# Kernel optimization log

Measured on AMD Instinct MI355X. Metric: run time of the kernel, lower is better.

## Reference

```python
import jax, jax.numpy as jnp
import numpy as np

N, E, ND, ED, H, L = 50000, 800000, 64, 32, 128, 4
MIN = 2 * H + H + 1  # message MLP input dim = 385
EPS = 1e-5


def _layernorm(x, w, b):
    mu = x.mean(-1, keepdims=True)
    var = ((x - mu) ** 2).mean(-1, keepdims=True)
    return (x - mu) / jnp.sqrt(var + EPS) * w + b


def setup_inputs() -> dict:
    key = jax.random.key(0)
    ks = jax.random.split(key, 40)

    def w(k, shape):
        return jax.random.normal(k, shape, jnp.float32) / np.sqrt(shape[-2]).astype(np.float32)

    inp = {
        "node_features": jax.random.normal(ks[0], (N, ND), jnp.float32),
        "edge_features": jax.random.normal(ks[1], (E, ED), jnp.float32),
        "congestion": jax.random.uniform(ks[2], (N,), jnp.float32),
        "edge_index": jax.random.randint(ks[3], (2, E), 0, N),
        "unrouted_mask": jax.random.randint(ks[4], (N,), 0, 2).astype(jnp.bool_),
        "enc_node_w": w(ks[5], (ND, H)), "enc_node_b": jnp.zeros(H),
        "enc_edge_w": w(ks[6], (ED, H)), "enc_edge_b": jnp.zeros(H),
        "msg_w1": w(ks[7], (L, MIN, H)), "msg_b1": jnp.zeros((L, H)),
        "msg_w2": w(ks[8], (L, H, H)), "msg_b2": jnp.zeros((L, H)),
        "upd_w1": w(ks[9], (L, 2 * H, H)), "upd_b1": jnp.zeros((L, H)),
        "upd_w2": w(ks[10], (L, H, H)), "upd_b2": jnp.zeros((L, H)),
        "ln_w": jnp.ones((L, H)), "ln_b": jnp.zeros((L, H)),
        "unr_w1": w(ks[11], (1, H)), "unr_b1": jnp.zeros(H),
        "unr_w2": w(ks[12], (H, H)), "unr_b2": jnp.zeros(H),
        "ro_w1": w(ks[13], (2 * H, H)), "ro_b1": jnp.zeros(H),
        "ro_w2": w(ks[14], (H, H // 2)), "ro_b2": jnp.zeros(H // 2),
        "ro_w3": w(ks[15], (H // 2, 1)), "ro_b3": jnp.zeros(1),
    }
    return inp


def reference(node_features, edge_features, congestion, edge_index, unrouted_mask,
              enc_node_w, enc_node_b, enc_edge_w, enc_edge_b,
              msg_w1, msg_b1, msg_w2, msg_b2,
              upd_w1, upd_b1, upd_w2, upd_b2,
              ln_w, ln_b,
              unr_w1, unr_b1, unr_w2, unr_b2,
              ro_w1, ro_b1, ro_w2, ro_b2, ro_w3, ro_b3):
    n = node_features.shape[0]
    src, dst = edge_index[0], edge_index[1]

    x = node_features @ enc_node_w + enc_node_b            # [N, H]
    ea = edge_features @ enc_edge_w + enc_edge_b           # [E, H]
    cong_src = congestion[src][:, None]                    # [E, 1]

    for l in range(msg_w1.shape[0]):
        # message: gather src/dst features, concat with edge attr + congestion
        m_in = jnp.concatenate([x[src], x[dst], ea, cong_src], axis=-1)  # [E, 385]
        m = jax.nn.relu(m_in @ msg_w1[l] + msg_b1[l]) @ msg_w2[l] + msg_b2[l]  # [E, H]
        agg = jax.ops.segment_sum(m, dst, num_segments=n)  # scatter_add over dst
        u_in = jnp.concatenate([x, agg], axis=-1)          # [N, 2H]
        x_new = jax.nn.relu(u_in @ upd_w1[l] + upd_b1[l]) @ upd_w2[l] + upd_b2[l]
        x = _layernorm(x + x_new, ln_w[l], ln_b[l])        # dropout = identity (eval)

    graph_embed = x.mean(axis=0, keepdims=True)            # [1, H] (batch=None branch)
    unrouted_frac = unrouted_mask.astype(jnp.float32).mean()[None, None]  # [1, 1]
    unr = jax.nn.relu(unrouted_frac @ unr_w1 + unr_b1) @ unr_w2 + unr_b2  # [1, H]
    combined = jnp.concatenate([graph_embed, unr], axis=-1)  # [1, 2H]
    h = jax.nn.relu(combined @ ro_w1 + ro_b1)
    h = jax.nn.relu(h @ ro_w2 + ro_b2)
    out = jax.nn.sigmoid(h @ ro_w3 + ro_b3)                # [1, 1]
    return out.squeeze(-1)                                 # [1]
```

## Files before the change

### kernel.cpp

```cpp
#include <hip/hip_runtime.h>
#include <hip/hip_fp16.h>
#include <math.h>

#define NN 50000
#define EE 800000

typedef _Float16 half8 __attribute__((ext_vector_type(8)));
typedef __fp16 fp16x2 __attribute__((ext_vector_type(2)));
typedef float floatx4 __attribute__((ext_vector_type(4)));

__global__ void fold_kernel(const float* __restrict__ ew, const float* __restrict__ eb,
                            const float* __restrict__ w1, const float* __restrict__ b1,
                            float* __restrict__ Wc, float* __restrict__ b1f) {
  int l = blockIdx.y, c = blockIdx.x, j = threadIdx.x;
  __shared__ float row[128];
  const float* w1l = w1 + (size_t)l * 385 * 128;
  if (c < 32) {
    row[j] = ew[c * 128 + j];
    __syncthreads();
    float acc = 0.f;
    for (int k = 0; k < 128; k++) acc += row[k] * w1l[(256 + k) * 128 + j];
    Wc[((size_t)l * 32 + c) * 128 + j] = acc;
  } else {
    row[j] = eb[j];
    __syncthreads();
    float acc = b1[l * 128 + j];
    for (int k = 0; k < 128; k++) acc += row[k] * w1l[(256 + k) * 128 + j];
    b1f[l * 128 + j] = acc;
  }
}

__global__ void prep_w(const float* __restrict__ src, _Float16* __restrict__ dst,
                       int K, int perm) {
  int l = blockIdx.y;
  int lane = threadIdx.x;
  int kc = blockIdx.x >> 3, nt = blockIdx.x & 7;
  int n = nt * 16 + (lane & 15);
  int k0 = kc * 32 + (lane >> 4) * 8;
  const float* s = src + (size_t)l * K * 128;
  _Float16 out[8];
  for (int j = 0; j < 8; j++) {
    int k = k0 + j;
    int ks = perm ? ((k & 7) * 16 + (k >> 3)) : k;
    out[j] = (_Float16)s[(size_t)ks * 128 + n];
  }
  _Float16* d = dst + (((size_t)l * gridDim.x + blockIdx.x) * 64 + lane) * 8;
  *(half8*)d = *(half8*)out;
}

__global__ void prep_cong(const float* __restrict__ mw1, _Float16* __restrict__ w1cp) {
  int l = blockIdx.x, p = threadIdx.x;
  int col = (p & 7) * 16 + (p >> 3);
  w1cp[l * 128 + p] = (_Float16)mw1[((size_t)l * 385 + 384) * 128 + col];
}

__global__ void hist_kernel(const int* __restrict__ dstv, int* __restrict__ counts,
                            int* __restrict__ rank) {
  int e = blockIdx.x * 256 + threadIdx.x;
  if (e < EE) rank[e] = atomicAdd(&counts[dstv[e]], 1);
}

__global__ void scan1_kernel(const int* __restrict__ counts, int* __restrict__ offs,
                             int* __restrict__ bsum) {
  __shared__ int ws[16];
  int t = threadIdx.x, lane = t & 63, w = t >> 6;
  int i = blockIdx.x * 1024 + t;
  int v = (i < NN) ? counts[i] : 0;
  int s = v;
  for (int off = 1; off < 64; off <<= 1) {
    int u = __shfl_up(s, off);
    if (lane >= off) s += u;
  }
  if (lane == 63) ws[w] = s;
  __syncthreads();
  if (w == 0) {
    int u = (lane < 16) ? ws[lane] : 0;
    for (int off = 1; off < 16; off <<= 1) {
      int x = __shfl_up(u, off);
      if (lane >= off && lane < 16) u += x;
    }
    if (lane < 16) ws[lane] = u;
  }
  __syncthreads();
  int wbase = (w > 0) ? ws[w - 1] : 0;
  if (i < NN) offs[i] = wbase + s - v;
  if (t == 0) bsum[blockIdx.x] = ws[15];
}

__global__ void scan2_kernel(int* __restrict__ bsum) {
  int t = threadIdx.x;
  int v = (t < 49) ? bsum[t] : 0;
  int s = v;
  for (int off = 1; off < 64; off <<= 1) {
    int u = __shfl_up(s, off);
    if (t >= off) s += u;
  }
  if (t < 49) bsum[t] = s - v;
}

__global__ void slot1_kernel(const int* __restrict__ dstv, const int* __restrict__ offs,
                             const int* __restrict__ bsum, const int* __restrict__ rank,
                             int* __restrict__ einv) {
  int e = blockIdx.x * 256 + threadIdx.x;
  if (e >= EE) return;
  int d = dstv[e];
  int p = offs[d] + bsum[d >> 10] + rank[e];
  einv[p] = e;
}

__global__ void slot2_kernel(const int* __restrict__ einv, const int* __restrict__ srcv,
                             const int* __restrict__ dstv, const float* __restrict__ ef,
                             int2* __restrict__ meta, _Float16* __restrict__ efh) {
  int p = blockIdx.x * 256 + threadIdx.x;
  if (p >= EE) return;
  int e = einv[p];
  int2 m;
  m.x = srcv[e];
  m.y = dstv[e];
  meta[p] = m;
  const float* sp = ef + (size_t)e * 32;
  _Float16* dp = efh + (size_t)p * 32;
  for (int i = 0; i < 4; i++) {
    float4 f = *(const float4*)(sp + i * 8);
    float4 g = *(const float4*)(sp + i * 8 + 4);
    half8 v;
    v[0] = (_Float16)f.x; v[1] = (_Float16)f.y; v[2] = (_Float16)f.z; v[3] = (_Float16)f.w;
    v[4] = (_Float16)g.x; v[5] = (_Float16)g.y; v[6] = (_Float16)g.z; v[7] = (_Float16)g.w;
    *(half8*)(dp + i * 8) = v;
  }
}

__global__ void enc_mfma(const float* __restrict__ nf, const _Float16* __restrict__ Wenc,
                         const float* __restrict__ bn, _Float16* __restrict__ xh,
                         const _Float16* __restrict__ WSa, const _Float16* __restrict__ WSb,
                         const float* __restrict__ b1f,
                         _Float16* __restrict__ Sh, _Float16* __restrict__ Dh,
                         _Float16* __restrict__ aggz,
                         const int* __restrict__ um, float* __restrict__ red) {
  __shared__ __align__(16) _Float16 hs[4][16][136];
  int t = threadIdx.x, wave = t >> 6, lane = t & 63;
  int quad = lane >> 4, l15 = lane & 15;
  long nb0 = (long)blockIdx.x * 64 + wave * 16;
  long rn = nb0 + l15;
  if (rn >= NN) rn = NN - 1;

  {
    long zn = (long)blockIdx.x * 64 + (t >> 2);
    if (zn < NN) {
      float4* p = (float4*)(aggz + (long)blockIdx.x * 64 * 128 + t * 32);
      float4 z = {};
      p[0] = z; p[1] = z; p[2] = z; p[3] = z;
    }
  }

  if (t < 64) {
    long n = (long)blockIdx.x * 64 + t;
    float mv = (n < NN) ? (float)um[n] : 0.f;
    for (int off = 32; off; off >>= 1) mv += __shfl_xor(mv, off);
    if (t == 0) atomicAdd(&red[128], mv);
  }

  floatx4 acc[8] = {};
  for (int kc = 0; kc < 2; kc++) {
    const float* p = nf + rn * 64 + kc * 32 + quad * 8;
    float4 f0 = *(const float4*)p;
    float4 f1 = *(const float4*)(p + 4);
    half8 a;
    a[0] = (_Float16)f0.x; a[1] = (_Float16)f0.y;
    a[2] = (_Float16)f0.z; a[3] = (_Float16)f0.w;
    a[4] = (_Float16)f1.x; a[5] = (_Float16)f1.y;
    a[6] = (_Float16)f1.z; a[7] = (_Float16)f1.w;
    const _Float16* bp = Wenc + (size_t)(kc * 8) * 512 + lane * 8;
    for (int nt = 0; nt < 8; nt++) {
      half8 b = *(const half8*)(bp + nt * 512);
      acc[nt] = __builtin_amdgcn_mfma_f32_16x16x32_f16(a, b, acc[nt], 0, 0, 0);
    }
  }
  float bv[8];
  for (int nt = 0; nt < 8; nt++) bv[nt] = bn[nt * 16 + l15];
  for (int reg = 0; reg < 4; reg++) {
    long n = nb0 + quad * 4 + reg;
    bool ok = n < NN;
    for (int nt = 0; nt < 8; nt++) {
      _Float16 v = (_Float16)(acc[nt][reg] + bv[nt]);
      if (ok) xh[n * 128 + nt * 16 + l15] = v;
      hs[wave][quad * 4 + reg][nt * 16 + l15] = v;
    }
  }

  {
    floatx4 as_[8] = {}, ad[8] = {};
#pragma unroll
    for (int kc = 0; kc < 4; kc++) {
      half8 a = *(const half8*)&hs[wave][l15][kc * 32 + quad * 8];
      const _Float16* bpa = WSa + (size_t)(kc * 8) * 512 + lane * 8;
      const _Float16* bpb = WSb + (size_t)(kc * 8) * 512 + lane * 8;
#pragma unroll
      for (int nt = 0; nt < 8; nt++) {
        half8 ba = *(const half8*)(bpa + nt * 512);
        half8 bbq = *(const half8*)(bpb + nt * 512);
        as_[nt] = __builtin_amdgcn_mfma_f32_16x16x32_f16(a, ba, as_[nt], 0, 0, 0);
        ad[nt] = __builtin_amdgcn_mfma_f32_16x16x32_f16(a, bbq, ad[nt], 0, 0, 0);
      }
    }
    float bfv[8];
    for (int nt = 0; nt < 8; nt++) bfv[nt] = b1f[nt * 16 + l15];
    for (int reg = 0; reg < 4; reg++) {
      long n = nb0 + quad * 4 + reg;
      if (n < NN) {
        half8 hsv, hdv;
        for (int nt = 0; nt < 8; nt++) {
          hsv[nt] = (_Float16)as_[nt][reg];
          hdv[nt] = (_Float16)(ad[nt][reg] + bfv[nt]);
        }
        *(half8*)(Sh + n * 128 + l15 * 8) = hsv;
        *(half8*)(Dh + n * 128 + l15 * 8) = hdv;
      }
    }
  }
}

__global__ __launch_bounds__(128, 3) void msg_kernel(
    const _Float16* __restrict__ Sh, const _Float16* __restrict__ Dh,
    const _Float16* __restrict__ efh, const int2* __restrict__ meta,
    const float* __restrict__ cong,
    const _Float16* __restrict__ Wcp, const _Float16* __restrict__ Wp2,
    const _Float16* __restrict__ w1cp, const float* __restrict__ b2,
    __half* __restrict__ agg) {
  __shared__ __align__(16) _Float16 As[64][136];
  __shared__ int s_src[64], s_dst[64];
  __shared__ float s_cg[64];
  int t = threadIdx.x, wave = t >> 6, lane = t & 63;
  int quad = lane >> 4, l15 = lane & 15;
  long eb0 = (long)blockIdx.x * 64;
  int web = wave * 32;

  if (t < 64) {
    int2 m = meta[eb0 + t];
    s_src[t] = m.x;
    s_dst[t] = m.y;
    s_cg[t] = cong[m.x];
  }
  half8 wcl = *(const half8*)(w1cp + l15 * 8);
  half8 av0 = *(const half8*)(efh + (size_t)(eb0 + web + l15) * 32 + quad * 8);
  half8 av1 = *(const half8*)(efh + (size_t)(eb0 + web + 16 + l15) * 32 + quad * 8);
  __syncthreads();

  half8 sv[8], dv[8];
#pragma unroll
  for (int mtl = 0; mtl < 2; mtl++)
#pragma unroll
    for (int reg = 0; reg < 4; reg++) {
      int r = web + mtl * 16 + quad * 4 + reg;
      sv[mtl * 4 + reg] = *(const half8*)(Sh + (size_t)s_src[r] * 128 + l15 * 8);
      dv[mtl * 4 + reg] = *(const half8*)(Dh + (size_t)s_dst[r] * 128 + l15 * 8);
    }

#pragma unroll
  for (int mtl = 0; mtl < 2; mtl++) {
    half8 a = mtl ? av1 : av0;
    floatx4 e[8] = {};
#pragma unroll
    for (int nt = 0; nt < 8; nt++) {
      half8 b = *(const half8*)(Wcp + (size_t)nt * 512 + lane * 8);
      e[nt] = __builtin_amdgcn_mfma_f32_16x16x32_f16(a, b, e[nt], 0, 0, 0);
    }
#pragma unroll
    for (int reg = 0; reg < 4; reg++) {
      int r = web + mtl * 16 + quad * 4 + reg;
      _Float16 cgh = (_Float16)s_cg[r];
      half8 v = sv[mtl * 4 + reg] + dv[mtl * 4 + reg];
      half8 e8;
#pragma unroll
      for (int i = 0; i < 4; i++) {
        fp16x2 p = __builtin_amdgcn_cvt_pkrtz(e[2 * i][reg], e[2 * i + 1][reg]);
        e8[2 * i] = (_Float16)p[0];
        e8[2 * i + 1] = (_Float16)p[1];
      }
      v += e8;
      v += wcl * cgh;
#pragma unroll
      for (int i = 0; i < 8; i++) v[i] = v[i] > (_Float16)0 ? v[i] : (_Float16)0;
      *(half8*)&As[r][l15 * 8] = v;
    }
  }
  __syncthreads();

  int nb = wave * 4;
  floatx4 acc2[4][4] = {};
  __builtin_amdgcn_s_setprio(1);
#pragma unroll
  for (int kc = 0; kc < 4; kc++) {
    const _Float16* bp = Wp2 + ((size_t)(kc * 8 + nb)) * 512 + lane * 8;
    half8 b0 = *(const half8*)bp;
    half8 b1v = *(const half8*)(bp + 512);
    half8 b2v = *(const half8*)(bp + 1024);
    half8 b3v = *(const half8*)(bp + 1536);
#pragma unroll
    for (int mt = 0; mt < 4; mt++) {
      half8 a = *(const half8*)&As[mt * 16 + l15][kc * 32 + quad * 8];
      acc2[mt][0] = __builtin_amdgcn_mfma_f32_16x16x32_f16(a, b0, acc2[mt][0], 0, 0, 0);
      acc2[mt][1] = __builtin_amdgcn_mfma_f32_16x16x32_f16(a, b1v, acc2[mt][1], 0, 0, 0);
      acc2[mt][2] = __builtin_amdgcn_mfma_f32_16x16x32_f16(a, b2v, acc2[mt][2], 0, 0, 0);
      acc2[mt][3] = __builtin_amdgcn_mfma_f32_16x16x32_f16(a, b3v, acc2[mt][3], 0, 0, 0);
    }
  }
  __builtin_amdgcn_s_setprio(0);
  __syncthreads();

  {
    float c[4];
#pragma unroll
    for (int ntp = 0; ntp < 4; ntp++) c[ntp] = b2[(nb + ntp) * 16 + l15];
#pragma unroll
    for (int mt = 0; mt < 4; mt++)
#pragma unroll
      for (int reg = 0; reg < 4; reg++) {
        int row = mt * 16 + quad * 4 + reg;
#pragma unroll
        for (int ntp = 0; ntp < 4; ntp++)
          As[row][(nb + ntp) * 16 + l15] = (_Float16)(acc2[mt][ntp][reg] + c[ntp]);
      }
  }
  __syncthreads();

  {
    int cp = lane;
    int r0 = wave * 32;
    __half2 vals[32];
#pragma unroll
    for (int i = 0; i < 32; i++) vals[i] = *(__half2*)&As[r0 + i][cp * 2];
    int cur = s_dst[r0];
    __half2 acc = __float2half2_rn(0.f);
    for (int i = 0; i < 32; i++) {
      int d = s_dst[r0 + i];
      if (d != cur) {
        unsafeAtomicAdd((__half2*)(agg + (long)cur * 128 + cp * 2), acc);
        acc = __float2half2_rn(0.f);
        cur = d;
      }
      acc = __hadd2(acc, vals[i]);
    }
    unsafeAtomicAdd((__half2*)(agg + (long)cur * 128 + cp * 2), acc);
  }
}

template <bool DO_RED>
__global__ __launch_bounds__(256, 3) void upd_kernel(
    _Float16* __restrict__ xh, _Float16* __restrict__ agg,
    const _Float16* __restrict__ Wp1, const _Float16* __restrict__ Wp2,
    const float* __restrict__ b1, const float* __restrict__ b2,
    const float* __restrict__ g, const float* __restrict__ bb,
    const _Float16* __restrict__ WSa, const _Float16* __restrict__ WSb,
    const float* __restrict__ b1f,
    _Float16* __restrict__ Sh, _Float16* __restrict__ Dh,
    float* __restrict__ red) {
  __shared__ __align__(16) _Float16 hs[4][16][136];
  int t = threadIdx.x, wave = t >> 6, lane = t & 63;
  int quad = lane >> 4, l15 = lane & 15;
  long nb0 = (long)blockIdx.x * 64 + wave * 16;

  floatx4 acc[8] = {};
  {
    long n = nb0 + l15;
    long rn = n < NN ? n : NN - 1;
    for (int kc = 0; kc < 8; kc++) {
      half8 a;
      if (kc < 4) {
        a = *(const half8*)(xh + rn * 128 + kc * 32 + quad * 8);
      } else {
        a = *(const half8*)(agg + rn * 128 + (kc - 4) * 32 + quad * 8);
      }
      const _Float16* bp = Wp1 + (size_t)(kc * 8) * 512 + lane * 8;
      for (int nt = 0; nt < 8; nt++) {
        half8 b = *(const half8*)(bp + nt * 512);
        acc[nt] = __builtin_amdgcn_mfma_f32_16x16x32_f16(a, b, acc[nt], 0, 0, 0);
      }
    }
  }

  float bbv[8];
  for (int nt = 0; nt < 8; nt++) bbv[nt] = b1[nt * 16 + l15];
  for (int reg = 0; reg < 4; reg++) {
    half8 hv;
    for (int nt = 0; nt < 8; nt++)
      hv[nt] = (_Float16)fmaxf(acc[nt][reg] + bbv[nt], 0.f);
    *(half8*)&hs[wave][quad * 4 + reg][l15 * 8] = hv;
  }
  __syncthreads();

  floatx4 acc2[8] = {};
  for (int kc = 0; kc < 4; kc++) {
    half8 a = *(const half8*)&hs[wave][l15][kc * 32 + quad * 8];
    const _Float16* bp = Wp2 + (size_t)(kc * 8) * 512 + lane * 8;
    for (int nt = 0; nt < 8; nt++) {
      half8 b = *(const half8*)(bp + nt * 512);
      acc2[nt] = __builtin_amdgcn_mfma_f32_16x16x32_f16(a, b, acc2[nt], 0, 0, 0);
    }
  }

  float b2v[8], gv[8], bv[8];
  for (int nt = 0; nt < 8; nt++) {
    int col = nt * 16 + l15;
    b2v[nt] = b2[col]; gv[nt] = g[col]; bv[nt] = bb[col];
  }
  bool fuse = (WSa != nullptr);
  float cs[DO_RED ? 8 : 1];
  if (DO_RED)
    for (int nt = 0; nt < (DO_RED ? 8 : 1); nt++) cs[nt] = 0.f;
  for (int reg = 0; reg < 4; reg++) {
    long n = nb0 + quad * 4 + reg;
    bool ok = n < NN;
    long rn = ok ? n : NN - 1;
    float y[8];
    float s = 0.f;
    for (int nt = 0; nt < 8; nt++) {
      y[nt] = (float)xh[rn * 128 + nt * 16 + l15] + acc2[nt][reg] + b2v[nt];
      s += y[nt];
    }
    s += __shfl_xor(s, 1); s += __shfl_xor(s, 2);
    s += __shfl_xor(s, 4); s += __shfl_xor(s, 8);
    float mu = s * (1.f / 128.f);
    float q = 0.f;
    for (int nt = 0; nt < 8; nt++) {
      y[nt] -= mu;
      q += y[nt] * y[nt];
    }
    q += __shfl_xor(q, 1); q += __shfl_xor(q, 2);
    q += __shfl_xor(q, 4); q += __shfl_xor(q, 8);
    float rstd = rsqrtf(q * (1.f / 128.f) + 1e-5f);
    for (int nt = 0; nt < 8; nt++) {
      _Float16 o = (_Float16)(y[nt] * rstd * gv[nt] + bv[nt]);
      if (ok) xh[n * 128 + nt * 16 + l15] = o;
      if (fuse) hs[wave][quad * 4 + reg][nt * 16 + l15] = o;
      if (DO_RED) cs[nt] += ok ? (float)o : 0.f;
    }
  }

  if (fuse) {
    floatx4 as_[8] = {}, ad[8] = {};
#pragma unroll
    for (int kc = 0; kc < 4; kc++) {
      half8 a = *(const half8*)&hs[wave][l15][kc * 32 + quad * 8];
      const _Float16* bpa = WSa + (size_t)(kc * 8) * 512 + lane * 8;
      const _Float16* bpb = WSb + (size_t)(kc * 8) * 512 + lane * 8;
#pragma unroll
      for (int nt = 0; nt < 8; nt++) {
        half8 ba = *(const half8*)(bpa + nt * 512);
        half8 bbq = *(const half8*)(bpb + nt * 512);
        as_[nt] = __builtin_amdgcn_mfma_f32_16x16x32_f16(a, ba, as_[nt], 0, 0, 0);
        ad[nt] = __builtin_amdgcn_mfma_f32_16x16x32_f16(a, bbq, ad[nt], 0, 0, 0);
      }
    }
    float bfv[8];
    for (int nt = 0; nt < 8; nt++) bfv[nt] = b1f[nt * 16 + l15];
    for (int reg = 0; reg < 4; reg++) {
      long n = nb0 + quad * 4 + reg;
      if (n < NN) {
        half8 hsv, hdv;
        for (int nt = 0; nt < 8; nt++) {
          hsv[nt] = (_Float16)as_[nt][reg];
          hdv[nt] = (_Float16)(ad[nt][reg] + bfv[nt]);
        }
        *(half8*)(Sh + n * 128 + l15 * 8) = hsv;
        *(half8*)(Dh + n * 128 + l15 * 8) = hdv;
      }
    }

    long zn = (long)blockIdx.x * 64 + (t >> 2);
    if (zn < NN) {
      float4* p = (float4*)(agg + (long)blockIdx.x * 64 * 128 + t * 32);
      float4 z = {};
      p[0] = z; p[1] = z; p[2] = z; p[3] = z;
    }
  }

  if (DO_RED) {
    for (int nt = 0; nt < 8; nt++) {
      cs[nt] += __shfl_xor(cs[nt], 16);
      cs[nt] += __shfl_xor(cs[nt], 32);
    }
    __syncthreads();
    float* hsF = (float*)hs;
    if (quad == 0)
      for (int nt = 0; nt < 8; nt++) hsF[wave * 128 + nt * 16 + l15] = cs[nt];
    __syncthreads();
    if (t < 128)
      atomicAdd(&red[t], hsF[t] + hsF[128 + t] + hsF[256 + t] + hsF[384 + t]);
  }
}

__global__ void readout_kernel(const float* __restrict__ red,
                               const float* __restrict__ xw1, const float* __restrict__ xb1,
                               const float* __restrict__ xw2, const float* __restrict__ xb2,
                               const float* __restrict__ rw1, const float* __restrict__ rb1,
                               const float* __restrict__ rw2, const float* __restrict__ rb2,
                               const float* __restrict__ rw3, const float* __restrict__ rb3,
                               float* __restrict__ out) {
  __shared__ float sa[128], sb[128], sc[128];
  int j = threadIdx.x;
  const float inv = 1.f / (float)NN;
  float ge = red[j] * inv;
  float uf = red[128] * inv;
  float u1 = fmaxf(uf * xw1[j] + xb1[j], 0.f);
  sa[j] = u1;
  sb[j] = ge;
  __syncthreads();
  float u2 = xb2[j];
  for (int k = 0; k < 128; k++) u2 += sa[k] * xw2[k * 128 + j];
  sc[j] = u2;
  __syncthreads();
  float h1 = rb1[j];
  for (int k = 0; k < 128; k++) h1 += sb[k] * rw1[k * 128 + j];
  for (int k = 0; k < 128; k++) h1 += sc[k] * rw1[(128 + k) * 128 + j];
  h1 = fmaxf(h1, 0.f);
  __syncthreads();
  sa[j] = h1;
  __syncthreads();
  float h2 = 0.f;
  if (j < 64) {
    h2 = rb2[j];
    for (int k = 0; k < 128; k++) h2 += sa[k] * rw2[k * 64 + j];
    h2 = fmaxf(h2, 0.f);
  }
  __syncthreads();
  if (j < 64) sb[j] = h2;
  __syncthreads();
  if (j == 0) {
    float a = rb3[0];
    for (int k = 0; k < 64; k++) a += sb[k] * rw3[k];
    out[0] = 1.f / (1.f + expf(-a));
  }
}

extern "C" void kernel_launch(void* const* d_in, const int* in_sizes, int n_in,
                              void* d_out, int out_size, void* d_ws, size_t ws_size,
                              hipStream_t stream) {
  const float* nf   = (const float*)d_in[0];
  const float* ef   = (const float*)d_in[1];
  const float* cong = (const float*)d_in[2];
  const int*   eidx = (const int*)d_in[3];
  const int*   um   = (const int*)d_in[4];
  const float* enw  = (const float*)d_in[5];
  const float* enb  = (const float*)d_in[6];
  const float* eew  = (const float*)d_in[7];
  const float* eeb  = (const float*)d_in[8];
  const float* mw1  = (const float*)d_in[9];
  const float* mb1  = (const float*)d_in[10];
  const float* mw2  = (const float*)d_in[11];
  const float* mb2  = (const float*)d_in[12];
  const float* uw1  = (const float*)d_in[13];
  const float* ub1  = (const float*)d_in[14];
  const float* uw2  = (const float*)d_in[15];
  const float* ub2  = (const float*)d_in[16];
  const float* lnw  = (const float*)d_in[17];
  const float* lnb  = (const float*)d_in[18];
  const float* xw1  = (const float*)d_in[19];
  const float* xb1  = (const float*)d_in[20];
  const float* xw2  = (const float*)d_in[21];
  const float* xb2  = (const float*)d_in[22];
  const float* rw1  = (const float*)d_in[23];
  const float* rb1  = (const float*)d_in[24];
  const float* rw2  = (const float*)d_in[25];
  const float* rb2  = (const float*)d_in[26];
  const float* rw3  = (const float*)d_in[27];
  const float* rb3  = (const float*)d_in[28];
  float* out = (float*)d_out;

  char* W = (char*)d_ws;
  _Float16* xh    = (_Float16*)(W + 0);
  __half*   agg   = (__half*)(W + 12800000);
  _Float16* efh   = (_Float16*)(W + 25600000);
  _Float16* Sh    = (_Float16*)(W + 76800000);
  _Float16* Dh    = (_Float16*)(W + 89600000);
  int2*     meta  = (int2*)(W + 102400000);
  int*      einv  = (int*)(W + 108800000);
  int*      counts= (int*)(W + 112000000);
  int*      offs  = (int*)(W + 112400000);
  _Float16* WSa   = (_Float16*)(W + 112600000);
  _Float16* WSb   = (_Float16*)(W + 112731072);
  _Float16* Wcp   = (_Float16*)(W + 112862144);
  _Float16* Wm2   = (_Float16*)(W + 112894912);
  _Float16* Wu1   = (_Float16*)(W + 113025984);
  _Float16* Wu2   = (_Float16*)(W + 113288128);
  _Float16* Wen   = (_Float16*)(W + 113419200);
  float*    Wc    = (float*)(W + 113435584);
  float*    b1f   = (float*)(W + 113501120);
  _Float16* w1cp  = (_Float16*)(W + 113503168);
  float*    red   = (float*)(W + 113504192);
  int*      rank  = (int*)meta;
  int*      bsum  = (int*)red;

  const int* srcv = eidx;
  const int* dstv = eidx + EE;

  (void)hipMemsetAsync(counts, 0, 200000, stream);
  hist_kernel<<<3125, 256, 0, stream>>>(dstv, counts, rank);
  scan1_kernel<<<49, 1024, 0, stream>>>(counts, offs, bsum);
  scan2_kernel<<<1, 64, 0, stream>>>(bsum);
  slot1_kernel<<<3125, 256, 0, stream>>>(dstv, offs, bsum, rank, einv);
  slot2_kernel<<<3125, 256, 0, stream>>>(einv, srcv, dstv, ef, meta, efh);

  fold_kernel<<<dim3(33, 4), 128, 0, stream>>>(eew, eeb, mw1, mb1, Wc, b1f);
  prep_w<<<dim3(8, 4), 64, 0, stream>>>(Wc, Wcp, 32, 0);
  prep_w<<<dim3(32, 4), 64, 0, stream>>>(mw1, WSa, 385, 0);
  prep_w<<<dim3(32, 4), 64, 0, stream>>>(mw1 + 128 * 128, WSb, 385, 0);
  prep_w<<<dim3(32, 4), 64, 0, stream>>>(mw2, Wm2, 128, 1);
  prep_w<<<dim3(64, 4), 64, 0, stream>>>(uw1, Wu1, 256, 0);
  prep_w<<<dim3(32, 4), 64, 0, stream>>>(uw2, Wu2, 128, 1);
  prep_w<<<dim3(16, 1), 64, 0, stream>>>(enw, Wen, 64, 0);
  prep_cong<<<4, 128, 0, stream>>>(mw1, w1cp);
  (void)hipMemsetAsync(red, 0, 129 * sizeof(float), stream);
  enc_mfma<<<782, 256, 0, stream>>>(nf, Wen, enb, xh, WSa, WSb, b1f, Sh, Dh,
                                    (_Float16*)agg, um, red);

  for (int l = 0; l < 4; l++) {
    msg_kernel<<<12500, 128, 0, stream>>>(
        Sh, Dh, efh, meta, cong,
        Wcp + (size_t)l * 8 * 512, Wm2 + (size_t)l * 32 * 512,
        w1cp + l * 128, mb2 + l * 128, agg);
    if (l < 3) {
      upd_kernel<false><<<782, 256, 0, stream>>>(
          xh, (_Float16*)agg,
          Wu1 + (size_t)l * 64 * 512, Wu2 + (size_t)l * 32 * 512,
          ub1 + l * 128, ub2 + l * 128, lnw + l * 128, lnb + l * 128,
          WSa + (size_t)(l + 1) * 32 * 512, WSb + (size_t)(l + 1) * 32 * 512,
          b1f + (l + 1) * 128, Sh, Dh, red);
    } else {
      upd_kernel<true><<<782, 256, 0, stream>>>(
          xh, (_Float16*)agg,
          Wu1 + (size_t)l * 64 * 512, Wu2 + (size_t)l * 32 * 512,
          ub1 + l * 128, ub2 + l * 128, lnw + l * 128, lnb + l * 128,
          (const _Float16*)nullptr, (const _Float16*)nullptr,
          (const float*)nullptr, Sh, Dh, red);
    }
  }

  readout_kernel<<<1, 128, 0, stream>>>(red, xw1, xb1, xw2, xb2,
                                        rw1, rb1, rw2, rb2, rw3, rb3, out);
}
```

Baseline: 803.5 us.

## Merge weight prep launches, batch slot2 loads, reuse x tile in update

Replaces eight separate weight-conversion launches with a single prep_all kernel that dispatches on block index, cutting launch overhead. slot2_kernel now handles two edges per thread and issues all feature loads before the conversions and stores, to raise memory-level parallelism. upd_kernel stages the x rows it already loads for the first GEMM into shared memory and reads them back for the residual, instead of re-reading xh from global. The extra LDS buffer raises shared memory per block, which may reduce occupancy.

```diff
diff --git a/kernel.cpp b/kernel.cpp
--- a/kernel.cpp
+++ b/kernel.cpp
@@ -30,11 +30,11 @@
   }
 }
 
-__global__ void prep_w(const float* __restrict__ src, _Float16* __restrict__ dst,
-                       int K, int perm) {
-  int l = blockIdx.y;
-  int lane = threadIdx.x;
-  int kc = blockIdx.x >> 3, nt = blockIdx.x & 7;
+__device__ __forceinline__ void prep_body(const float* __restrict__ src,
+                                          _Float16* __restrict__ dst,
+                                          int K, int perm, int gx, int l,
+                                          int bx, int lane) {
+  int kc = bx >> 3, nt = bx & 7;
   int n = nt * 16 + (lane & 15);
   int k0 = kc * 32 + (lane >> 4) * 8;
   const float* s = src + (size_t)l * K * 128;
@@ -44,14 +44,40 @@
     int ks = perm ? ((k & 7) * 16 + (k >> 3)) : k;
     out[j] = (_Float16)s[(size_t)ks * 128 + n];
   }
-  _Float16* d = dst + (((size_t)l * gridDim.x + blockIdx.x) * 64 + lane) * 8;
+  _Float16* d = dst + (((size_t)l * gx + bx) * 64 + lane) * 8;
   *(half8*)d = *(half8*)out;
 }
 
-__global__ void prep_cong(const float* __restrict__ mw1, _Float16* __restrict__ w1cp) {
-  int l = blockIdx.x, p = threadIdx.x;
-  int col = (p & 7) * 16 + (p >> 3);
-  w1cp[l * 128 + p] = (_Float16)mw1[((size_t)l * 385 + 384) * 128 + col];
+__global__ void prep_all(const float* __restrict__ mw1, const float* __restrict__ mw2,
+                         const float* __restrict__ uw1, const float* __restrict__ uw2,
+                         const float* __restrict__ enw, const float* __restrict__ Wc,
+                         _Float16* __restrict__ WSa, _Float16* __restrict__ WSb,
+                         _Float16* __restrict__ Wm2, _Float16* __restrict__ Wu1,
+                         _Float16* __restrict__ Wu2, _Float16* __restrict__ Wcp,
+                         _Float16* __restrict__ Wen, _Float16* __restrict__ w1cp) {
+  int b = blockIdx.x, lane = threadIdx.x;
+  if (b < 128) {
+    prep_body(mw1, WSa, 385, 0, 32, b >> 5, b & 31, lane);
+  } else if (b < 256) {
+    b -= 128; prep_body(mw1 + 128 * 128, WSb, 385, 0, 32, b >> 5, b & 31, lane);
+  } else if (b < 384) {
+    b -= 256; prep_body(mw2, Wm2, 128, 1, 32, b >> 5, b & 31, lane);
+  } else if (b < 640) {
+    b -= 384; prep_body(uw1, Wu1, 256, 0, 64, b >> 6, b & 63, lane);
+  } else if (b < 768) {
+    b -= 640; prep_body(uw2, Wu2, 128, 1, 32, b >> 5, b & 31, lane);
+  } else if (b < 800) {
+    b -= 768; prep_body(Wc, Wcp, 32, 0, 8, b >> 3, b & 7, lane);
+  } else if (b < 816) {
+    b -= 800; prep_body(enw, Wen, 64, 0, 16, 0, b, lane);
+  } else {
+    int l = b - 816;
+    for (int h = 0; h < 2; h++) {
+      int p = lane + h * 64;
+      int col = (p & 7) * 16 + (p >> 3);
+      w1cp[l * 128 + p] = (_Float16)mw1[((size_t)l * 385 + 384) * 128 + col];
+    }
+  }
 }
 
 __global__ void hist_kernel(const int* __restrict__ dstv, int* __restrict__ counts,
@@ -111,22 +137,47 @@
 __global__ void slot2_kernel(const int* __restrict__ einv, const int* __restrict__ srcv,
                              const int* __restrict__ dstv, const float* __restrict__ ef,
                              int2* __restrict__ meta, _Float16* __restrict__ efh) {
-  int p = blockIdx.x * 256 + threadIdx.x;
-  if (p >= EE) return;
-  int e = einv[p];
-  int2 m;
-  m.x = srcv[e];
-  m.y = dstv[e];
-  meta[p] = m;
-  const float* sp = ef + (size_t)e * 32;
-  _Float16* dp = efh + (size_t)p * 32;
-  for (int i = 0; i < 4; i++) {
-    float4 f = *(const float4*)(sp + i * 8);
-    float4 g = *(const float4*)(sp + i * 8 + 4);
-    half8 v;
-    v[0] = (_Float16)f.x; v[1] = (_Float16)f.y; v[2] = (_Float16)f.z; v[3] = (_Float16)f.w;
-    v[4] = (_Float16)g.x; v[5] = (_Float16)g.y; v[6] = (_Float16)g.z; v[7] = (_Float16)g.w;
-    *(half8*)(dp + i * 8) = v;
+  int p0 = blockIdx.x * 512 + threadIdx.x;
+  int p1 = p0 + 256;
+  bool v0 = p0 < EE, v1 = p1 < EE;
+  int e0 = v0 ? einv[p0] : 0;
+  int e1 = v1 ? einv[p1] : 0;
+  int s0 = v0 ? srcv[e0] : 0, d0 = v0 ? dstv[e0] : 0;
+  int s1 = v1 ? srcv[e1] : 0, d1 = v1 ? dstv[e1] : 0;
+  const float* sp0 = ef + (size_t)e0 * 32;
+  const float* sp1 = ef + (size_t)e1 * 32;
+  float4 f0[8], f1[8];
+#pragma unroll
+  for (int i = 0; i < 8; i++) f0[i] = *(const float4*)(sp0 + i * 4);
+#pragma unroll
+  for (int i = 0; i < 8; i++) f1[i] = *(const float4*)(sp1 + i * 4);
+  if (v0) {
+    int2 m; m.x = s0; m.y = d0;
+    meta[p0] = m;
+    _Float16* dp = efh + (size_t)p0 * 32;
+#pragma unroll
+    for (int i = 0; i < 4; i++) {
+      half8 v;
+      v[0] = (_Float16)f0[2*i].x; v[1] = (_Float16)f0[2*i].y;
+      v[2] = (_Float16)f0[2*i].z; v[3] = (_Float16)f0[2*i].w;
+      v[4] = (_Float16)f0[2*i+1].x; v[5] = (_Float16)f0[2*i+1].y;
+      v[6] = (_Float16)f0[2*i+1].z; v[7] = (_Float16)f0[2*i+1].w;
+      *(half8*)(dp + i * 8) = v;
+    }
+  }
+  if (v1) {
+    int2 m; m.x = s1; m.y = d1;
+    meta[p1] = m;
+    _Float16* dp = efh + (size_t)p1 * 32;
+#pragma unroll
+    for (int i = 0; i < 4; i++) {
+      half8 v;
+      v[0] = (_Float16)f1[2*i].x; v[1] = (_Float16)f1[2*i].y;
+      v[2] = (_Float16)f1[2*i].z; v[3] = (_Float16)f1[2*i].w;
+      v[4] = (_Float16)f1[2*i+1].x; v[5] = (_Float16)f1[2*i+1].y;
+      v[6] = (_Float16)f1[2*i+1].z; v[7] = (_Float16)f1[2*i+1].w;
+      *(half8*)(dp + i * 8) = v;
+    }
   }
 }
 
@@ -356,6 +407,7 @@
     _Float16* __restrict__ Sh, _Float16* __restrict__ Dh,
     float* __restrict__ red) {
   __shared__ __align__(16) _Float16 hs[4][16][136];
+  __shared__ __align__(16) _Float16 xs[4][16][136];
   int t = threadIdx.x, wave = t >> 6, lane = t & 63;
   int quad = lane >> 4, l15 = lane & 15;
   long nb0 = (long)blockIdx.x * 64 + wave * 16;
@@ -368,6 +420,7 @@
       half8 a;
       if (kc < 4) {
         a = *(const half8*)(xh + rn * 128 + kc * 32 + quad * 8);
+        *(half8*)&xs[wave][l15][kc * 32 + quad * 8] = a;
       } else {
         a = *(const half8*)(agg + rn * 128 + (kc - 4) * 32 + quad * 8);
       }
@@ -411,11 +464,11 @@
   for (int reg = 0; reg < 4; reg++) {
     long n = nb0 + quad * 4 + reg;
     bool ok = n < NN;
-    long rn = ok ? n : NN - 1;
     float y[8];
     float s = 0.f;
     for (int nt = 0; nt < 8; nt++) {
-      y[nt] = (float)xh[rn * 128 + nt * 16 + l15] + acc2[nt][reg] + b2v[nt];
+      y[nt] = (float)xs[wave][quad * 4 + reg][nt * 16 + l15] +
+              acc2[nt][reg] + b2v[nt];
       s += y[nt];
     }
     s += __shfl_xor(s, 1); s += __shfl_xor(s, 2);
@@ -599,17 +652,11 @@
   scan1_kernel<<<49, 1024, 0, stream>>>(counts, offs, bsum);
   scan2_kernel<<<1, 64, 0, stream>>>(bsum);
   slot1_kernel<<<3125, 256, 0, stream>>>(dstv, offs, bsum, rank, einv);
-  slot2_kernel<<<3125, 256, 0, stream>>>(einv, srcv, dstv, ef, meta, efh);
+  slot2_kernel<<<1563, 256, 0, stream>>>(einv, srcv, dstv, ef, meta, efh);
 
   fold_kernel<<<dim3(33, 4), 128, 0, stream>>>(eew, eeb, mw1, mb1, Wc, b1f);
-  prep_w<<<dim3(8, 4), 64, 0, stream>>>(Wc, Wcp, 32, 0);
-  prep_w<<<dim3(32, 4), 64, 0, stream>>>(mw1, WSa, 385, 0);
-  prep_w<<<dim3(32, 4), 64, 0, stream>>>(mw1 + 128 * 128, WSb, 385, 0);
-  prep_w<<<dim3(32, 4), 64, 0, stream>>>(mw2, Wm2, 128, 1);
-  prep_w<<<dim3(64, 4), 64, 0, stream>>>(uw1, Wu1, 256, 0);
-  prep_w<<<dim3(32, 4), 64, 0, stream>>>(uw2, Wu2, 128, 1);
-  prep_w<<<dim3(16, 1), 64, 0, stream>>>(enw, Wen, 64, 0);
-  prep_cong<<<4, 128, 0, stream>>>(mw1, w1cp);
+  prep_all<<<820, 64, 0, stream>>>(mw1, mw2, uw1, uw2, enw, Wc,
+                                   WSa, WSb, Wm2, Wu1, Wu2, Wcp, Wen, w1cp);
   (void)hipMemsetAsync(red, 0, 129 * sizeof(float), stream);
   enc_mfma<<<782, 256, 0, stream>>>(nf, Wen, enb, xh, WSa, WSb, b1f, Sh, Dh,
                                     (_Float16*)agg, um, red);
```

New measurement: 783.2 us. 2.5% less time.
